# Kernel optimization log

Measured on AMD Instinct MI355X. Metric: run time of the kernel, lower is better.

The kernel has to match this reference:

```python
import jax, jax.numpy as jnp
import numpy as np

B, T, N = 2048, 48, 32
DYN, STAT, H = 6, 5, 64
IN = DYN + STAT


def setup_inputs() -> dict:
    key = jax.random.key(0)
    ks = jax.random.split(key, 18)
    rn = lambda k, s: jax.random.normal(k, s, jnp.float32) * 0.05
    return {
        "x_history": jax.random.normal(ks[0], (B, T, N, IN), jnp.float32),
        "adj": jax.random.uniform(ks[1], (N, N), dtype=jnp.float32),
        "W_enc": rn(ks[2], (IN, H)), "b_enc": jnp.zeros((H,), jnp.float32),
        "W_g1": rn(ks[3], (H, H)), "b_g1": jnp.zeros((H,), jnp.float32),
        "W_g2": rn(ks[4], (H, H)), "b_g2": jnp.zeros((H,), jnp.float32),
        "W_ih": rn(ks[5], (4 * H, H)), "W_hh": rn(ks[6], (4 * H, H)),
        "b_ih": jnp.zeros((4 * H,), jnp.float32), "b_hh": jnp.zeros((4 * H,), jnp.float32),
        "W_d1": rn(ks[7], (H, H // 2)), "b_d1": jnp.zeros((H // 2,), jnp.float32),
        "W_d2": rn(ks[8], (H // 2, DYN)), "b_d2": jnp.zeros((DYN,), jnp.float32),
        "future_steps": 48,
    }


def _norm_adj(adj):
    # PyG DenseGCNConv: set self-loops to 1, symmetric D^-1/2 (A) D^-1/2
    n = adj.shape[0]
    a = adj.at[jnp.diag_indices(n)].set(1.0)
    d = jnp.clip(a.sum(-1), 1.0) ** -0.5
    return d[:, None] * a * d[None, :]


def reference(x_history, adj, W_enc, b_enc, W_g1, b_g1, W_g2, b_g2,
              W_ih, W_hh, b_ih, b_hh, W_d1, b_d1, W_d2, b_d2, future_steps):
    b, t, n, _ = x_history.shape
    h = W_enc.shape[1]
    dyn = W_d2.shape[1]
    Ahat = _norm_adj(adj)

    def spatial(x):  # x: [b, n, in] -> [b*n, h]
        enc = jax.nn.relu(x @ W_enc + b_enc)
        s = jax.nn.relu(jnp.einsum('ij,bjh->bih', Ahat, enc @ W_g1) + b_g1)
        s = jax.nn.relu(jnp.einsum('ij,bjh->bih', Ahat, s @ W_g2) + b_g2)
        return s.reshape(b * n, h)

    def lstm(xf, hx, cx):  # torch LSTMCell gate order: i, f, g, o
        g = xf @ W_ih.T + b_ih + hx @ W_hh.T + b_hh
        gi, gf, gg, go = jnp.split(g, 4, axis=-1)
        c = jax.nn.sigmoid(gf) * cx + jax.nn.sigmoid(gi) * jnp.tanh(gg)
        return jax.nn.sigmoid(go) * jnp.tanh(c), c

    hx = jnp.zeros((b * n, h), x_history.dtype)
    cx = jnp.zeros((b * n, h), x_history.dtype)

    def enc_step(carry, x_t):
        hx, cx = carry
        hx, cx = lstm(spatial(x_t), hx, cx)
        return (hx, cx), None

    (hx, cx), _ = jax.lax.scan(enc_step, (hx, cx), jnp.swapaxes(x_history, 0, 1))

    last = x_history[:, -1]  # [b, n, in]
    pred = last[..., :dyn]
    stat = last[..., dyn:]

    def dec_step(carry, _):
        pred, hx, cx = carry
        cur = jnp.concatenate([pred, stat], axis=-1)
        hx, cx = lstm(spatial(cur), hx, cx)
        hu = hx.reshape(b, n, h)
        res = jax.nn.relu(hu @ W_d1 + b_d1) @ W_d2 + b_d2
        pred = pred + res
        return (pred, hx, cx), pred

    _, outs = jax.lax.scan(dec_step, (pred, hx, cx), None, length=future_steps)
    return jnp.swapaxes(outs, 0, 1)  # [b, future_steps, n, dyn]
```

## Files before the change

kernel.cpp:

```cpp
#include <hip/hip_runtime.h>
#include <cstdint>


#define NT 512
#define TSTEPS 48
#define FUT 48

typedef __bf16 bf16;
typedef __attribute__((ext_vector_type(2))) __bf16 bf16x2;
typedef __attribute__((ext_vector_type(8))) __bf16 bf16x8;
typedef __attribute__((ext_vector_type(16))) float f32x16;
typedef unsigned int uint32x4v __attribute__((ext_vector_type(4)));

__device__ __forceinline__ float sigm(float x) {
  return __builtin_amdgcn_rcpf(1.0f + __builtin_amdgcn_exp2f(x * -1.442695041f));
}
__device__ __forceinline__ float tanh_fast(float x) {
  return __builtin_fmaf(-2.0f,
           __builtin_amdgcn_rcpf(1.0f + __builtin_amdgcn_exp2f(x * 2.885390082f)),
           1.0f);
}

__device__ __forceinline__ uint32_t pk2(float x, float y) {
  union { bf16x2 h; uint32_t u; } t;
  t.h[0] = (bf16)x; t.h[1] = (bf16)y;
  return t.u;
}

__device__ __forceinline__ bf16x8 cpack8(float v0, float v1, float v2, float v3,
                                         float v4, float v5, float v6, float v7) {
  uint32_t a0 = pk2(v0, v1), a1 = pk2(v2, v3);
  uint32_t b0 = pk2(v4, v5), b1 = pk2(v6, v7);
  auto r0 = __builtin_amdgcn_permlane32_swap(a0, b0, false, false);
  auto r1 = __builtin_amdgcn_permlane32_swap(a1, b1, false, false);
  union { uint32x4v u; bf16x8 h; } o;
  o.u = uint32x4v{(uint32_t)r0[0], (uint32_t)r1[0], (uint32_t)r0[1], (uint32_t)r1[1]};
  return o.h;
}

__global__ __launch_bounds__(NT, 2)
void stgnn_kernel(const float* __restrict__ xh, const float* __restrict__ adj,
                  const float* __restrict__ Wenc, const float* __restrict__ benc,
                  const float* __restrict__ Wg1, const float* __restrict__ bg1,
                  const float* __restrict__ Wg2, const float* __restrict__ bg2,
                  const float* __restrict__ Wih, const float* __restrict__ Whh,
                  const float* __restrict__ bih, const float* __restrict__ bhh,
                  const float* __restrict__ Wd1, const float* __restrict__ bd1,
                  const float* __restrict__ Wd2, const float* __restrict__ bd2,
                  float* __restrict__ out) {
  __shared__ __align__(16) bf16 wcatTA[32768];
  __shared__ __align__(16) bf16 wg1B[4096];
  __shared__ __align__(16) bf16 wg2B[4096];
  __shared__ __align__(16) bf16 wencTA[1024];
  __shared__ __align__(16) bf16 wd1TA[2048];
  __shared__ __align__(16) bf16 wd2TA[1024];
  __shared__ __align__(16) bf16 ahHiB[1024];
  __shared__ __align__(16) bf16 ahLoB[1024];
  __shared__ __align__(16) float sBenc[64];
  __shared__ __align__(16) float sBg1[64];
  __shared__ __align__(16) float sBg2[64];
  __shared__ __align__(16) float sBih[256];
  __shared__ __align__(16) float sBd1[32];
  __shared__ __align__(16) float sBd2[8];
  __shared__ float sDeg[32];
  __shared__ __align__(16) float sAh[1024];
  __shared__ __align__(16) bf16 sXbA[8 * 512];

  const int tid = threadIdx.x;
  const int L   = tid & 63;
  const int w   = tid >> 6;
  const int n5  = L & 31;
  const int hf  = L >> 5;
  const long long b = (long long)blockIdx.x * 8 + w;

  bf16* sXb = sXbA + (w << 9);

  for (int i = tid; i < 1024; i += NT) {
    int f = i >> 6, h = i & 63;
    float v = (f < 11) ? Wenc[f * 64 + h] : 0.0f;
    wencTA[(h >> 5) * 512 + ((h & 31) + 32 * ((f >> 3) & 1)) * 8 + (f & 7)] = (bf16)v;
  }
  for (int i = tid; i < 4096; i += NT) {
    int k = i >> 6, n = i & 63;
    int off = (((n >> 5) * 4 + (k >> 4)) * 64 + (n & 31) + 32 * ((k >> 3) & 1)) * 8 + (k & 7);
    wg1B[off] = (bf16)Wg1[i];
    wg2B[off] = (bf16)Wg2[i];
  }
  for (int i = tid; i < 32768; i += NT) {
    int gc = i >> 7, k = i & 127;
    float v = (k < 64) ? Wih[gc * 64 + k] : Whh[gc * 64 + (k - 64)];
    wcatTA[((gc >> 5) * 8 + (k >> 4)) * 512 + ((gc & 31) + 32 * ((k >> 3) & 1)) * 8 + (k & 7)] = (bf16)v;
  }
  for (int i = tid; i < 2048; i += NT) {
    int k = i >> 5, n = i & 31;
    wd1TA[(k >> 4) * 512 + (n + 32 * ((k >> 3) & 1)) * 8 + (k & 7)] = (bf16)Wd1[k * 32 + n];
  }
  for (int i = tid; i < 1024; i += NT) {
    int k = i >> 5, d = i & 31;
    float v = (d < 6) ? Wd2[k * 6 + d] : 0.0f;
    wd2TA[(k >> 4) * 512 + (d + 32 * ((k >> 3) & 1)) * 8 + (k & 7)] = (bf16)v;
  }
  for (int i = tid; i < 64; i += NT) { sBenc[i] = benc[i]; sBg1[i] = bg1[i]; sBg2[i] = bg2[i]; }
  for (int i = tid; i < 256; i += NT) sBih[i] = bih[i] + bhh[i];
  for (int i = tid; i < 32; i += NT) sBd1[i] = bd1[i];
  if (tid < 8) sBd2[tid] = (tid < 6) ? bd2[tid] : 0.0f;
  if (tid < 32) {
    float s = 0.0f;
    for (int j = 0; j < 32; ++j) s += (j == tid) ? 1.0f : adj[tid * 32 + j];
    sDeg[tid] = 1.0f / sqrtf(fmaxf(s, 1.0f));
  }
  __syncthreads();
  for (int i = tid; i < 1024; i += NT) {
    int ii = i >> 5, jj = i & 31;
    float v = (ii == jj) ? 1.0f : adj[i];
    sAh[i] = sDeg[ii] * v * sDeg[jj];
  }
  __syncthreads();
  if (w == 0) {
    #pragma unroll
    for (int c = 0; c < 2; ++c)
      #pragma unroll
      for (int j = 0; j < 8; ++j) {
        int k = 16 * c + 8 * hf + j;
        float v = sAh[n5 * 32 + k];
        bf16 hi = (bf16)v;
        ahHiB[c * 512 + L * 8 + j] = hi;
        ahLoB[c * 512 + L * 8 + j] = (bf16)(v - (float)hi);
      }
  }
  __syncthreads();

  const bf16x8 aH0 = *reinterpret_cast<const bf16x8*>(&ahHiB[L * 8]);
  const bf16x8 aL0 = *reinterpret_cast<const bf16x8*>(&ahLoB[L * 8]);
  const bf16x8 aH1 = *reinterpret_cast<const bf16x8*>(&ahHiB[512 + L * 8]);
  const bf16x8 aL1 = *reinterpret_cast<const bf16x8*>(&ahLoB[512 + L * 8]);
  const bf16x8 wencR0 = *reinterpret_cast<const bf16x8*>(&wencTA[L * 8]);
  const bf16x8 wencR1 = *reinterpret_cast<const bf16x8*>(&wencTA[512 + L * 8]);

  float cx[32];
  #pragma unroll
  for (int i = 0; i < 32; ++i) cx[i] = 0.0f;
  bf16x8 xfhB[8];
  #pragma unroll
  for (int t = 0; t < 8; ++t)
    #pragma unroll
    for (int j = 0; j < 8; ++j) xfhB[t][j] = (bf16)0.0f;
  float predr[4] = {0.f, 0.f, 0.f, 0.f};
  float st0 = 0.f, st1 = 0.f, st2 = 0.f;

  for (int i = L; i < 512; i += 64) sXb[i] = (bf16)0.0f;
  float xpre[6];
  #pragma unroll
  for (int t = 0; t < 6; ++t) {
    int i = L + (t << 6);
    xpre[t] = (i < 352) ? xh[b * (TSTEPS * 352) + i] : 0.0f;
  }
  #pragma unroll
  for (int t = 0; t < 6; ++t) {
    int i = L + (t << 6);
    if (i < 352) { int j = i / 11, f = i - j * 11; sXb[(j << 4) + f] = (bf16)xpre[t]; }
  }
  #pragma unroll
  for (int t = 0; t < 6; ++t) {
    int i = L + (t << 6);
    if (i < 352) xpre[t] = xh[b * (TSTEPS * 352) + 352 + i];
  }
  bf16x8 xBcur = *reinterpret_cast<const bf16x8*>(&sXb[(n5 << 4) + (hf << 3)]);

  #pragma unroll 1
  for (int step = 0; step < TSTEPS + FUT; ++step) {
    asm volatile("" ::: "memory");
    const bool de = (step >= TSTEPS);
    const bf16x8 xB = xBcur;
    if (!de) {
      if (step + 1 < TSTEPS) {
        #pragma unroll
        for (int t = 0; t < 6; ++t) {
          int i = L + (t << 6);
          if (i < 352) { int j = i / 11, f = i - j * 11; sXb[(j << 4) + f] = (bf16)xpre[t]; }
        }
      }
      if (step + 2 < TSTEPS) {
        #pragma unroll
        for (int t = 0; t < 6; ++t) {
          int i = L + (t << 6);
          if (i < 352) xpre[t] = xh[b * (TSTEPS * 352) + (step + 2) * 352 + i];
        }
      }
      xBcur = *reinterpret_cast<const bf16x8*>(&sXb[(n5 << 4) + (hf << 3)]);
    }
    bf16x8 rA[4];
    #pragma unroll
    for (int mt = 0; mt < 2; ++mt) {
      f32x16 c;
      #pragma unroll
      for (int g = 0; g < 4; ++g) {
        float4 bb = *reinterpret_cast<const float4*>(&sBenc[32 * mt + 8 * g + 4 * hf]);
        c[4*g+0] = bb.x; c[4*g+1] = bb.y; c[4*g+2] = bb.z; c[4*g+3] = bb.w;
      }
      c = __builtin_amdgcn_mfma_f32_32x32x16_bf16(mt ? wencR1 : wencR0, xB, c, 0, 0, 0);
      rA[2*mt]   = cpack8(fmaxf(c[0], 0.f), fmaxf(c[1], 0.f), fmaxf(c[2], 0.f), fmaxf(c[3], 0.f),
                          fmaxf(c[4], 0.f), fmaxf(c[5], 0.f), fmaxf(c[6], 0.f), fmaxf(c[7], 0.f));
      rA[2*mt+1] = cpack8(fmaxf(c[8], 0.f), fmaxf(c[9], 0.f), fmaxf(c[10], 0.f), fmaxf(c[11], 0.f),
                          fmaxf(c[12], 0.f), fmaxf(c[13], 0.f), fmaxf(c[14], 0.f), fmaxf(c[15], 0.f));
    }
    bf16x8 nA[4];
    #pragma unroll
    for (int nt = 0; nt < 2; ++nt) {
      f32x16 c;
      #pragma unroll
      for (int i = 0; i < 16; ++i) c[i] = 0.0f;
      #pragma unroll
      for (int cc = 0; cc < 4; ++cc)
        c = __builtin_amdgcn_mfma_f32_32x32x16_bf16(rA[cc],
              *reinterpret_cast<const bf16x8*>(&wg1B[(nt * 4 + cc) * 512 + L * 8]), c, 0, 0, 0);
      nA[2*nt]   = cpack8(c[0], c[1], c[2], c[3], c[4], c[5], c[6], c[7]);
      nA[2*nt+1] = cpack8(c[8], c[9], c[10], c[11], c[12], c[13], c[14], c[15]);
    }
    #pragma unroll
    for (int mt = 0; mt < 2; ++mt) {
      f32x16 c;
      #pragma unroll
      for (int g = 0; g < 4; ++g) {
        float4 bb = *reinterpret_cast<const float4*>(&sBg1[32 * mt + 8 * g + 4 * hf]);
        c[4*g+0] = bb.x; c[4*g+1] = bb.y; c[4*g+2] = bb.z; c[4*g+3] = bb.w;
      }
      c = __builtin_amdgcn_mfma_f32_32x32x16_bf16(nA[mt * 2 + 0], aH0, c, 0, 0, 0);
      c = __builtin_amdgcn_mfma_f32_32x32x16_bf16(nA[mt * 2 + 0], aL0, c, 0, 0, 0);
      c = __builtin_amdgcn_mfma_f32_32x32x16_bf16(nA[mt * 2 + 1], aH1, c, 0, 0, 0);
      c = __builtin_amdgcn_mfma_f32_32x32x16_bf16(nA[mt * 2 + 1], aL1, c, 0, 0, 0);
      rA[2*mt]   = cpack8(fmaxf(c[0], 0.f), fmaxf(c[1], 0.f), fmaxf(c[2], 0.f), fmaxf(c[3], 0.f),
                          fmaxf(c[4], 0.f), fmaxf(c[5], 0.f), fmaxf(c[6], 0.f), fmaxf(c[7], 0.f));
      rA[2*mt+1] = cpack8(fmaxf(c[8], 0.f), fmaxf(c[9], 0.f), fmaxf(c[10], 0.f), fmaxf(c[11], 0.f),
                          fmaxf(c[12], 0.f), fmaxf(c[13], 0.f), fmaxf(c[14], 0.f), fmaxf(c[15], 0.f));
    }
    #pragma unroll
    for (int nt = 0; nt < 2; ++nt) {
      f32x16 c;
      #pragma unroll
      for (int i = 0; i < 16; ++i) c[i] = 0.0f;
      #pragma unroll
      for (int cc = 0; cc < 4; ++cc)
        c = __builtin_amdgcn_mfma_f32_32x32x16_bf16(rA[cc],
              *reinterpret_cast<const bf16x8*>(&wg2B[(nt * 4 + cc) * 512 + L * 8]), c, 0, 0, 0);
      nA[2*nt]   = cpack8(c[0], c[1], c[2], c[3], c[4], c[5], c[6], c[7]);
      nA[2*nt+1] = cpack8(c[8], c[9], c[10], c[11], c[12], c[13], c[14], c[15]);
    }
    #pragma unroll
    for (int mt = 0; mt < 2; ++mt) {
      f32x16 c;
      #pragma unroll
      for (int g = 0; g < 4; ++g) {
        float4 bb = *reinterpret_cast<const float4*>(&sBg2[32 * mt + 8 * g + 4 * hf]);
        c[4*g+0] = bb.x; c[4*g+1] = bb.y; c[4*g+2] = bb.z; c[4*g+3] = bb.w;
      }
      c = __builtin_amdgcn_mfma_f32_32x32x16_bf16(nA[mt * 2 + 0], aH0, c, 0, 0, 0);
      c = __builtin_amdgcn_mfma_f32_32x32x16_bf16(nA[mt * 2 + 0], aL0, c, 0, 0, 0);
      c = __builtin_amdgcn_mfma_f32_32x32x16_bf16(nA[mt * 2 + 1], aH1, c, 0, 0, 0);
      c = __builtin_amdgcn_mfma_f32_32x32x16_bf16(nA[mt * 2 + 1], aL1, c, 0, 0, 0);
      xfhB[2*mt]   = cpack8(fmaxf(c[0], 0.f), fmaxf(c[1], 0.f), fmaxf(c[2], 0.f), fmaxf(c[3], 0.f),
                            fmaxf(c[4], 0.f), fmaxf(c[5], 0.f), fmaxf(c[6], 0.f), fmaxf(c[7], 0.f));
      xfhB[2*mt+1] = cpack8(fmaxf(c[8], 0.f), fmaxf(c[9], 0.f), fmaxf(c[10], 0.f), fmaxf(c[11], 0.f),
                            fmaxf(c[12], 0.f), fmaxf(c[13], 0.f), fmaxf(c[14], 0.f), fmaxf(c[15], 0.f));
    }
    bf16x8 hN[4];
    #pragma unroll
    for (int p = 0; p < 2; ++p) {
      f32x16 gI, gF, gG;
      #pragma unroll
      for (int g = 0; g < 4; ++g) {
        float4 bI = *reinterpret_cast<const float4*>(&sBih[      32 * p + 8 * g + 4 * hf]);
        float4 bF = *reinterpret_cast<const float4*>(&sBih[ 64 + 32 * p + 8 * g + 4 * hf]);
        float4 bG = *reinterpret_cast<const float4*>(&sBih[128 + 32 * p + 8 * g + 4 * hf]);
        gI[4*g+0]=bI.x; gI[4*g+1]=bI.y; gI[4*g+2]=bI.z; gI[4*g+3]=bI.w;
        gF[4*g+0]=bF.x; gF[4*g+1]=bF.y; gF[4*g+2]=bF.z; gF[4*g+3]=bF.w;
        gG[4*g+0]=bG.x; gG[4*g+1]=bG.y; gG[4*g+2]=bG.z; gG[4*g+3]=bG.w;
      }
      #pragma unroll
      for (int cc = 0; cc < 8; ++cc) {
        gI = __builtin_amdgcn_mfma_f32_32x32x16_bf16(
               *reinterpret_cast<const bf16x8*>(&wcatTA[((0 + p) * 8 + cc) * 512 + L * 8]),
               xfhB[cc], gI, 0, 0, 0);
        gF = __builtin_amdgcn_mfma_f32_32x32x16_bf16(
               *reinterpret_cast<const bf16x8*>(&wcatTA[((2 + p) * 8 + cc) * 512 + L * 8]),
               xfhB[cc], gF, 0, 0, 0);
        gG = __builtin_amdgcn_mfma_f32_32x32x16_bf16(
               *reinterpret_cast<const bf16x8*>(&wcatTA[((4 + p) * 8 + cc) * 512 + L * 8]),
               xfhB[cc], gG, 0, 0, 0);
      }
      float tc[16];
      #pragma unroll
      for (int ri = 0; ri < 16; ++ri) {
        float ccv = sigm(gF[ri]) * cx[p * 16 + ri] + sigm(gI[ri]) * tanh_fast(gG[ri]);
        cx[p * 16 + ri] = ccv;
        tc[ri] = tanh_fast(ccv);
      }
      f32x16 gO;
      #pragma unroll
      for (int g = 0; g < 4; ++g) {
        float4 bO = *reinterpret_cast<const float4*>(&sBih[192 + 32 * p + 8 * g + 4 * hf]);
        gO[4*g+0]=bO.x; gO[4*g+1]=bO.y; gO[4*g+2]=bO.z; gO[4*g+3]=bO.w;
      }
      #pragma unroll
      for (int cc = 0; cc < 8; ++cc)
        gO = __builtin_amdgcn_mfma_f32_32x32x16_bf16(
               *reinterpret_cast<const bf16x8*>(&wcatTA[((6 + p) * 8 + cc) * 512 + L * 8]),
               xfhB[cc], gO, 0, 0, 0);
      float hq[16];
      #pragma unroll
      for (int ri = 0; ri < 16; ++ri) hq[ri] = sigm(gO[ri]) * tc[ri];
      hN[2*p]   = cpack8(hq[0], hq[1], hq[2], hq[3], hq[4], hq[5], hq[6], hq[7]);
      hN[2*p+1] = cpack8(hq[8], hq[9], hq[10], hq[11], hq[12], hq[13], hq[14], hq[15]);
    }
    #pragma unroll
    for (int t = 0; t < 4; ++t) xfhB[4 + t] = hN[t];
    if (de) {
      if (step == TSTEPS) {
        const float* px = xh + ((b * TSTEPS + (TSTEPS - 1)) * 32 + n5) * 11;
        if (hf == 0) { predr[0] = px[0]; predr[1] = px[1]; predr[2] = px[2]; predr[3] = px[3]; }
        else         { predr[0] = px[4]; predr[1] = px[5]; }
        st0 = px[6 + 2 * hf]; st1 = px[7 + 2 * hf]; st2 = px[10];
      }
      f32x16 cD;
      #pragma unroll
      for (int g = 0; g < 4; ++g) {
        float4 bb = *reinterpret_cast<const float4*>(&sBd1[8 * g + 4 * hf]);
        cD[4*g+0] = bb.x; cD[4*g+1] = bb.y; cD[4*g+2] = bb.z; cD[4*g+3] = bb.w;
      }
      #pragma unroll
      for (int cc = 0; cc < 4; ++cc)
        cD = __builtin_amdgcn_mfma_f32_32x32x16_bf16(
               *reinterpret_cast<const bf16x8*>(&wd1TA[cc * 512 + L * 8]), xfhB[4 + cc], cD, 0, 0, 0);
      bf16x8 rB0 = cpack8(fmaxf(cD[0], 0.f), fmaxf(cD[1], 0.f), fmaxf(cD[2], 0.f), fmaxf(cD[3], 0.f),
                          fmaxf(cD[4], 0.f), fmaxf(cD[5], 0.f), fmaxf(cD[6], 0.f), fmaxf(cD[7], 0.f));
      bf16x8 rB1 = cpack8(fmaxf(cD[8], 0.f), fmaxf(cD[9], 0.f), fmaxf(cD[10], 0.f), fmaxf(cD[11], 0.f),
                          fmaxf(cD[12], 0.f), fmaxf(cD[13], 0.f), fmaxf(cD[14], 0.f), fmaxf(cD[15], 0.f));
      f32x16 c2;
      #pragma unroll
      for (int i = 0; i < 4; ++i) c2[i] = sBd2[4 * hf + i];
      #pragma unroll
      for (int i = 4; i < 16; ++i) c2[i] = 0.0f;
      c2 = __builtin_amdgcn_mfma_f32_32x32x16_bf16(
             *reinterpret_cast<const bf16x8*>(&wd2TA[L * 8]), rB0, c2, 0, 0, 0);
      c2 = __builtin_amdgcn_mfma_f32_32x32x16_bf16(
             *reinterpret_cast<const bf16x8*>(&wd2TA[512 + L * 8]), rB1, c2, 0, 0, 0);
      float* op = out + ((b * FUT + (step - TSTEPS)) * 32 + n5) * 6;
      if (hf == 0) {
        float p0 = predr[0] + c2[0];
        float p1 = predr[1] + c2[1];
        float p2 = predr[2] + c2[2];
        float p3 = predr[3] + c2[3];
        predr[0] = p0; predr[1] = p1; predr[2] = p2; predr[3] = p3;
        *reinterpret_cast<float2*>(op + 0) = make_float2(p0, p1);
        *reinterpret_cast<float2*>(op + 2) = make_float2(p2, p3);
      } else {
        float p4 = predr[0] + c2[0];
        float p5 = predr[1] + c2[1];
        predr[0] = p4; predr[1] = p5;
        *reinterpret_cast<float2*>(op + 4) = make_float2(p4, p5);
      }
      uint32_t pa = pk2(predr[0], predr[1]);
      auto sw = __builtin_amdgcn_permlane32_swap(pa, pa, false, false);
      uint32_t d0 = hf ? pk2(st0, st1)  : pa;
      uint32_t d1 = hf ? pk2(st2, 0.0f) : pk2(predr[2], predr[3]);
      uint32_t d2 = hf ? 0u : (uint32_t)sw[1];
      uint32_t d3 = hf ? 0u : pk2(st0, st1);
      union { uint32x4v u; bf16x8 h; } xo;
      xo.u = uint32x4v{d0, d1, d2, d3};
      xBcur = xo.h;
    }
  }
}

extern "C" void kernel_launch(void* const* d_in, const int* in_sizes, int n_in,
                              void* d_out, int out_size, void* d_ws, size_t ws_size,
                              hipStream_t stream) {
  (void)in_sizes; (void)n_in; (void)d_ws; (void)ws_size; (void)out_size;
  const float* xh   = (const float*)d_in[0];
  const float* adj  = (const float*)d_in[1];
  const float* Wenc = (const float*)d_in[2];
  const float* benc = (const float*)d_in[3];
  const float* Wg1  = (const float*)d_in[4];
  const float* bg1  = (const float*)d_in[5];
  const float* Wg2  = (const float*)d_in[6];
  const float* bg2  = (const float*)d_in[7];
  const float* Wih  = (const float*)d_in[8];
  const float* Whh  = (const float*)d_in[9];
  const float* bih  = (const float*)d_in[10];
  const float* bhh  = (const float*)d_in[11];
  const float* Wd1  = (const float*)d_in[12];
  const float* bd1  = (const float*)d_in[13];
  const float* Wd2  = (const float*)d_in[14];
  const float* bd2  = (const float*)d_in[15];
  float* out = (float*)d_out;
  stgnn_kernel<<<dim3(256), dim3(NT), 0, stream>>>(
      xh, adj, Wenc, benc, Wg1, bg1, Wg2, bg2,
      Wih, Whh, bih, bhh, Wd1, bd1, Wd2, bd2, out);
}
```

Measured before the change: 1.041 ms.

## Fold encoder bias into MFMA, hoist GCN weights to registers, merge LSTM reciprocals

Folds the encoder bias into the encoder MFMA by adding a constant-one input feature at column 11, which removes the shared-memory bias loads. Preloads the Wg1/Wg2 weight fragments into registers once, so the LDS reads inside each step go away. Rewrites the LSTM cell and hidden updates so the several sigmoid/tanh reciprocals collapse into one or two rcp calls per element. The costs are higher register pressure, possible overflow with large gate values in the merged formulas, and the encoder bias now being rounded to bf16.

```diff
diff --git a/kernel.cpp b/kernel.cpp
--- a/kernel.cpp
+++ b/kernel.cpp
@@ -12,14 +12,8 @@
 typedef __attribute__((ext_vector_type(16))) float f32x16;
 typedef unsigned int uint32x4v __attribute__((ext_vector_type(4)));
 
-__device__ __forceinline__ float sigm(float x) {
-  return __builtin_amdgcn_rcpf(1.0f + __builtin_amdgcn_exp2f(x * -1.442695041f));
-}
-__device__ __forceinline__ float tanh_fast(float x) {
-  return __builtin_fmaf(-2.0f,
-           __builtin_amdgcn_rcpf(1.0f + __builtin_amdgcn_exp2f(x * 2.885390082f)),
-           1.0f);
-}
+#define L2E  1.442695041f
+#define L2E2 2.885390082f
 
 __device__ __forceinline__ uint32_t pk2(float x, float y) {
   union { bf16x2 h; uint32_t u; } t;
@@ -56,7 +50,6 @@
   __shared__ __align__(16) bf16 wd2TA[1024];
   __shared__ __align__(16) bf16 ahHiB[1024];
   __shared__ __align__(16) bf16 ahLoB[1024];
-  __shared__ __align__(16) float sBenc[64];
   __shared__ __align__(16) float sBg1[64];
   __shared__ __align__(16) float sBg2[64];
   __shared__ __align__(16) float sBih[256];
@@ -77,7 +70,7 @@
 
   for (int i = tid; i < 1024; i += NT) {
     int f = i >> 6, h = i & 63;
-    float v = (f < 11) ? Wenc[f * 64 + h] : 0.0f;
+    float v = (f < 11) ? Wenc[f * 64 + h] : (f == 11 ? benc[h] : 0.0f);
     wencTA[(h >> 5) * 512 + ((h & 31) + 32 * ((f >> 3) & 1)) * 8 + (f & 7)] = (bf16)v;
   }
   for (int i = tid; i < 4096; i += NT) {
@@ -100,7 +93,7 @@
     float v = (d < 6) ? Wd2[k * 6 + d] : 0.0f;
     wd2TA[(k >> 4) * 512 + (d + 32 * ((k >> 3) & 1)) * 8 + (k & 7)] = (bf16)v;
   }
-  for (int i = tid; i < 64; i += NT) { sBenc[i] = benc[i]; sBg1[i] = bg1[i]; sBg2[i] = bg2[i]; }
+  for (int i = tid; i < 64; i += NT) { sBg1[i] = bg1[i]; sBg2[i] = bg2[i]; }
   for (int i = tid; i < 256; i += NT) sBih[i] = bih[i] + bhh[i];
   for (int i = tid; i < 32; i += NT) sBd1[i] = bd1[i];
   if (tid < 8) sBd2[tid] = (tid < 6) ? bd2[tid] : 0.0f;
@@ -136,6 +129,12 @@
   const bf16x8 aL1 = *reinterpret_cast<const bf16x8*>(&ahLoB[512 + L * 8]);
   const bf16x8 wencR0 = *reinterpret_cast<const bf16x8*>(&wencTA[L * 8]);
   const bf16x8 wencR1 = *reinterpret_cast<const bf16x8*>(&wencTA[512 + L * 8]);
+  bf16x8 wg1R[8], wg2R[8];
+  #pragma unroll
+  for (int c = 0; c < 8; ++c) {
+    wg1R[c] = *reinterpret_cast<const bf16x8*>(&wg1B[c * 512 + L * 8]);
+    wg2R[c] = *reinterpret_cast<const bf16x8*>(&wg2B[c * 512 + L * 8]);
+  }
 
   float cx[32];
   #pragma unroll
@@ -148,7 +147,7 @@
   float predr[4] = {0.f, 0.f, 0.f, 0.f};
   float st0 = 0.f, st1 = 0.f, st2 = 0.f;
 
-  for (int i = L; i < 512; i += 64) sXb[i] = (bf16)0.0f;
+  for (int i = L; i < 512; i += 64) sXb[i] = ((i & 15) == 11) ? (bf16)1.0f : (bf16)0.0f;
   float xpre[6];
   #pragma unroll
   for (int t = 0; t < 6; ++t) {
@@ -194,10 +193,7 @@
     for (int mt = 0; mt < 2; ++mt) {
       f32x16 c;
       #pragma unroll
-      for (int g = 0; g < 4; ++g) {
-        float4 bb = *reinterpret_cast<const float4*>(&sBenc[32 * mt + 8 * g + 4 * hf]);
-        c[4*g+0] = bb.x; c[4*g+1] = bb.y; c[4*g+2] = bb.z; c[4*g+3] = bb.w;
-      }
+      for (int i = 0; i < 16; ++i) c[i] = 0.0f;
       c = __builtin_amdgcn_mfma_f32_32x32x16_bf16(mt ? wencR1 : wencR0, xB, c, 0, 0, 0);
       rA[2*mt]   = cpack8(fmaxf(c[0], 0.f), fmaxf(c[1], 0.f), fmaxf(c[2], 0.f), fmaxf(c[3], 0.f),
                           fmaxf(c[4], 0.f), fmaxf(c[5], 0.f), fmaxf(c[6], 0.f), fmaxf(c[7], 0.f));
@@ -212,8 +208,7 @@
       for (int i = 0; i < 16; ++i) c[i] = 0.0f;
       #pragma unroll
       for (int cc = 0; cc < 4; ++cc)
-        c = __builtin_amdgcn_mfma_f32_32x32x16_bf16(rA[cc],
-              *reinterpret_cast<const bf16x8*>(&wg1B[(nt * 4 + cc) * 512 + L * 8]), c, 0, 0, 0);
+        c = __builtin_amdgcn_mfma_f32_32x32x16_bf16(rA[cc], wg1R[nt * 4 + cc], c, 0, 0, 0);
       nA[2*nt]   = cpack8(c[0], c[1], c[2], c[3], c[4], c[5], c[6], c[7]);
       nA[2*nt+1] = cpack8(c[8], c[9], c[10], c[11], c[12], c[13], c[14], c[15]);
     }
@@ -241,8 +236,7 @@
       for (int i = 0; i < 16; ++i) c[i] = 0.0f;
       #pragma unroll
       for (int cc = 0; cc < 4; ++cc)
-        c = __builtin_amdgcn_mfma_f32_32x32x16_bf16(rA[cc],
-              *reinterpret_cast<const bf16x8*>(&wg2B[(nt * 4 + cc) * 512 + L * 8]), c, 0, 0, 0);
+        c = __builtin_amdgcn_mfma_f32_32x32x16_bf16(rA[cc], wg2R[nt * 4 + cc], c, 0, 0, 0);
       nA[2*nt]   = cpack8(c[0], c[1], c[2], c[3], c[4], c[5], c[6], c[7]);
       nA[2*nt+1] = cpack8(c[8], c[9], c[10], c[11], c[12], c[13], c[14], c[15]);
     }
@@ -288,12 +282,17 @@
                *reinterpret_cast<const bf16x8*>(&wcatTA[((4 + p) * 8 + cc) * 512 + L * 8]),
                xfhB[cc], gG, 0, 0, 0);
       }
-      float tc[16];
       #pragma unroll
       for (int ri = 0; ri < 16; ++ri) {
-        float ccv = sigm(gF[ri]) * cx[p * 16 + ri] + sigm(gI[ri]) * tanh_fast(gG[ri]);
-        cx[p * 16 + ri] = ccv;
-        tc[ri] = tanh_fast(ccv);
+        float ef = __builtin_amdgcn_exp2f(gF[ri] * -L2E);
+        float ei = __builtin_amdgcn_exp2f(gI[ri] * -L2E);
+        float eg = __builtin_amdgcn_exp2f(gG[ri] * L2E2);
+        float D1 = 1.0f + ef;
+        float A  = 1.0f + ei;
+        float T  = __builtin_fmaf(A, eg, A);
+        float t1 = __builtin_fmaf(eg, D1, -D1);
+        float num = __builtin_fmaf(cx[p * 16 + ri], T, t1);
+        cx[p * 16 + ri] = num * __builtin_amdgcn_rcpf(D1 * T);
       }
       f32x16 gO;
       #pragma unroll
@@ -308,7 +307,13 @@
                xfhB[cc], gO, 0, 0, 0);
       float hq[16];
       #pragma unroll
-      for (int ri = 0; ri < 16; ++ri) hq[ri] = sigm(gO[ri]) * tc[ri];
+      for (int ri = 0; ri < 16; ++ri) {
+        float eo = __builtin_amdgcn_exp2f(gO[ri] * -L2E);
+        float ec = __builtin_amdgcn_exp2f(cx[p * 16 + ri] * L2E2);
+        float B1 = 1.0f + eo;
+        float T2 = __builtin_fmaf(B1, ec, B1);
+        hq[ri] = (ec - 1.0f) * __builtin_amdgcn_rcpf(T2);
+      }
       hN[2*p]   = cpack8(hq[0], hq[1], hq[2], hq[3], hq[4], hq[5], hq[6], hq[7]);
       hN[2*p+1] = cpack8(hq[8], hq[9], hq[10], hq[11], hq[12], hq[13], hq[14], hq[15]);
     }
@@ -362,7 +367,7 @@
       uint32_t pa = pk2(predr[0], predr[1]);
       auto sw = __builtin_amdgcn_permlane32_swap(pa, pa, false, false);
       uint32_t d0 = hf ? pk2(st0, st1)  : pa;
-      uint32_t d1 = hf ? pk2(st2, 0.0f) : pk2(predr[2], predr[3]);
+      uint32_t d1 = hf ? pk2(st2, 1.0f) : pk2(predr[2], predr[3]);
       uint32_t d2 = hf ? 0u : (uint32_t)sw[1];
       uint32_t d3 = hf ? 0u : pk2(st0, st1);
       union { uint32x4v u; bf16x8 h; } xo;
```

After: 945.6 us. 9.2% less time.
